# Kernel tuning notes

Hardware: AMD Instinct MI355X
Metric: run time of the kernel (lower is better)

The kernel has to match this reference:

```python
import jax, jax.numpy as jnp
import numpy as np

EMBED_DIM = 1024
B, T = 4, 2048

def setup_inputs() -> dict:
    key = jax.random.key(0)
    ks = jax.random.split(key, 7)
    s = 1.0 / np.sqrt(EMBED_DIM)
    return {
        "x": jax.random.normal(ks[0], (B, T, EMBED_DIM), dtype=jnp.float32),
        "Wq": jax.random.uniform(ks[1], (EMBED_DIM, EMBED_DIM), jnp.float32, -s, s),
        "bq": jax.random.uniform(ks[2], (EMBED_DIM,), jnp.float32, -s, s),
        "Wk": jax.random.uniform(ks[3], (EMBED_DIM, EMBED_DIM), jnp.float32, -s, s),
        "bk": jax.random.uniform(ks[4], (EMBED_DIM,), jnp.float32, -s, s),
        "Wv": jax.random.uniform(ks[5], (EMBED_DIM, EMBED_DIM), jnp.float32, -s, s),
        "bv": jax.random.uniform(ks[6], (EMBED_DIM,), jnp.float32, -s, s),
    }

def reference(x, Wq, bq, Wk, bk, Wv, bv):
    Bsz, Tlen, C = x.shape
    # torch Linear: y = x @ W.T + b
    Q = jnp.einsum('btc,dc->btd', x, Wq) + bq
    K = jnp.einsum('btc,dc->btd', x, Wk) + bk
    V = jnp.einsum('btc,dc->btd', x, Wv) + bv
    score = jnp.einsum('bqd,bkd->bqk', Q, K) / jnp.sqrt(jnp.float32(C))
    causal = jnp.tril(jnp.ones((Tlen, Tlen), dtype=bool))  # [T,T]
    score = jnp.where(causal, score, -jnp.inf)
    att = jax.nn.softmax(score, axis=-1)
    return jnp.einsum('bqk,bkd->bqd', att, V)
```

## Files before the change

kernel.cpp:

```cpp
#include <hip/hip_runtime.h>


using u16 = unsigned short;
typedef __attribute__((ext_vector_type(8))) short short8;
typedef __attribute__((ext_vector_type(4))) float f32x4;

__device__ __forceinline__ u16 f2b(float f) {
  unsigned u = __builtin_bit_cast(unsigned, f);
  u += 0x7fffu + ((u >> 16) & 1u);
  return (u16)(u >> 16);
}

__device__ __forceinline__ float b2f(u16 h) {
  return __builtin_bit_cast(float, (unsigned)h << 16);
}

__device__ __forceinline__ void async16(void* lds, const void* g) {
  __builtin_amdgcn_global_load_lds(
      (const __attribute__((address_space(1))) unsigned int*)g,
      (__attribute__((address_space(3))) unsigned int*)lds, 16, 0, 0);
}

__device__ __forceinline__ void block_barrier() {
  asm volatile("" ::: "memory");
  __builtin_amdgcn_s_barrier();
  asm volatile("" ::: "memory");
}

__global__ __launch_bounds__(256) void cvt_all_kernel(
    const float* __restrict__ x, const float* __restrict__ Wq,
    const float* __restrict__ Wk, const float* __restrict__ Wv,
    u16* __restrict__ xb, u16* __restrict__ Wcat) {
  const int i = blockIdx.x * 256 + threadIdx.x;
  const float* src;
  u16* dst;
  int c;
  if (i < 2097152) {
    src = x; dst = xb; c = i;
  } else {
    const int r = i - 2097152;
    const int seg = r >> 18;
    src = seg == 0 ? Wq : (seg == 1 ? Wk : Wv);
    dst = Wcat + (size_t)seg * 1048576;
    c = r & 262143;
  }
  const float4 v = reinterpret_cast<const float4*>(src)[c];
  ushort4 o;
  o.x = f2b(v.x); o.y = f2b(v.y); o.z = f2b(v.z); o.w = f2b(v.w);
  reinterpret_cast<ushort4*>(dst)[c] = o;
}

#define STG_A(buf, half, roff, ku)                                          \
  {                                                                         \
    async16(&Asm[buf][half][tid * 8], gA0 + (size_t)(roff)*lda + (ku));     \
    async16(&Asm[buf][half][4096 + tid * 8],                                \
            gA0 + (size_t)((roff) + 128) * lda + (ku));                     \
  }
#define STG_B(buf, half, roff, ku)                                          \
  {                                                                         \
    async16(&Bsm[buf][half][tid * 8], gB0 + (size_t)(roff)*ldb + (ku));     \
    async16(&Bsm[buf][half][4096 + tid * 8],                                \
            gB0 + (size_t)((roff) + 128) * ldb + (ku));                     \
  }
#define RD_A(buf, hh)                                                       \
  {                                                                         \
    _Pragma("unroll") for (int ii = 0; ii < 4; ++ii) {                      \
      a[ii][0] = *(const short8*)(&Asm[buf][hh][aoff + ii * 1024 + sk0]);   \
      a[ii][1] = *(const short8*)(&Asm[buf][hh][aoff + ii * 1024 + sk1]);   \
    }                                                                       \
  }
#define RD_B(buf, cc, breg)                                                 \
  {                                                                         \
    _Pragma("unroll") for (int jj = 0; jj < 2; ++jj) {                      \
      breg[jj][0] = *(const short8*)(&Bsm[buf][cc][boff + jj * 1024 + sk0]);\
      breg[jj][1] = *(const short8*)(&Bsm[buf][cc][boff + jj * 1024 + sk1]);\
    }                                                                       \
  }
#define QUAD(hh, cc, breg)                                                  \
  {                                                                         \
    __builtin_amdgcn_s_setprio(1);                                          \
    _Pragma("unroll") for (int ii = 0; ii < 4; ++ii)                        \
        _Pragma("unroll") for (int jj = 0; jj < 2; ++jj) {                  \
      acc[(hh)*4 + ii][(cc)*2 + jj] =                                       \
          __builtin_amdgcn_mfma_f32_16x16x32_bf16(                          \
              a[ii][0], breg[jj][0], acc[(hh)*4 + ii][(cc)*2 + jj], 0,0,0); \
      acc[(hh)*4 + ii][(cc)*2 + jj] =                                       \
          __builtin_amdgcn_mfma_f32_16x16x32_bf16(                          \
              a[ii][1], breg[jj][1], acc[(hh)*4 + ii][(cc)*2 + jj], 0,0,0); \
    }                                                                       \
    __builtin_amdgcn_s_setprio(0);                                          \
  }
#define LGK0 asm volatile("s_waitcnt lgkmcnt(0)" ::: "memory")
#define LGK8 asm volatile("s_waitcnt lgkmcnt(8)" ::: "memory")
#define VM6 asm volatile("s_waitcnt vmcnt(6)" ::: "memory")

template <int NT, typename Epi>
__device__ __forceinline__ void gemm256_8ph(const u16* __restrict__ A, int lda,
                                            const u16* __restrict__ B, int ldb,
                                            Epi&& epi) {
  __shared__ __align__(16) u16 Asm[2][2][8192];
  __shared__ __align__(16) u16 Bsm[2][2][8192];
  const int tid = threadIdx.x;
  const int lane = tid & 63;
  const int w = tid >> 6;
  const int wm = w >> 2;
  const int wn = w & 3;

  f32x4 acc[8][4];
#pragma unroll
  for (int i = 0; i < 8; ++i)
#pragma unroll
    for (int j = 0; j < 4; ++j) acc[i][j] = f32x4{0.f, 0.f, 0.f, 0.f};

  const int sr = tid >> 3;
  const int ce = ((tid & 7) ^ (sr & 7)) << 3;
  const u16* gA0 = A + (size_t)sr * lda + ce;
  const int bE = (sr & 31) + ((sr >> 5) << 6);
  const u16* gB0 = B + (size_t)bE * ldb + ce;

  const int l15 = lane & 15;
  const int hi = lane >> 4;
  const int lo7 = lane & 7;
  const int aoff = wm * 4096 + l15 * 64;
  const int boff = wn * 2048 + l15 * 64;
  const int sk0 = (hi ^ lo7) << 3;
  const int sk1 = ((4 + hi) ^ lo7) << 3;

  short8 a[4][2], bEr[2][2], bLr[2][2];

  STG_A(0, 0, 0, 0); STG_B(0, 0, 0, 0); STG_A(0, 1, 64, 0); STG_B(0, 1, 32, 0);
  STG_A(1, 0, 0, 64); STG_B(1, 0, 0, 64); STG_A(1, 1, 64, 64);
  VM6;
  block_barrier();

  for (int t = 0; t < NT; t += 2) {
    const int k1 = (t + 1) * 64;
    const int t2c = (t + 2 < NT) ? (t + 2) : (NT - 1);
    const int t3c = (t + 3 < NT) ? (t + 3) : (NT - 1);
    const int k2 = t2c * 64;
    const int k3 = t3c * 64;
    RD_A(0, 0); RD_B(0, 0, bEr); STG_B(1, 1, 32, k1); LGK8;
    block_barrier(); LGK0; QUAD(0, 0, bEr); block_barrier();
    RD_B(0, 1, bLr); STG_A(0, 0, 0, k2);
    block_barrier(); LGK0; QUAD(0, 1, bLr); block_barrier();
    RD_A(0, 1); STG_B(0, 0, 0, k2);
    block_barrier(); LGK0; QUAD(1, 1, bLr); block_barrier();
    STG_A(0, 1, 64, k2);
    VM6; block_barrier(); QUAD(1, 0, bEr); block_barrier();
    RD_A(1, 0); RD_B(1, 0, bEr); STG_B(0, 1, 32, k2); LGK8;
    block_barrier(); LGK0; QUAD(0, 0, bEr); block_barrier();
    RD_B(1, 1, bLr); STG_A(1, 0, 0, k3);
    block_barrier(); LGK0; QUAD(0, 1, bLr); block_barrier();
    RD_A(1, 1); STG_B(1, 0, 0, k3);
    block_barrier(); LGK0; QUAD(1, 1, bLr); block_barrier();
    STG_A(1, 1, 64, k3);
    VM6; block_barrier(); QUAD(1, 0, bEr); block_barrier();
  }
  asm volatile("s_waitcnt vmcnt(0)" ::: "memory");
  epi(acc, wm, wn, lane);
}

__global__ __launch_bounds__(512, 1) void qkv_qk_kernel(
    const u16* __restrict__ xb, const u16* __restrict__ Wcat,
    const float* __restrict__ bq, const float* __restrict__ bk,
    u16* __restrict__ Qb, u16* __restrict__ Kb) {
  const int bid = blockIdx.x;
  const int swz = (bid & 7) * 32 + (bid >> 3);
  const int mt = swz >> 3, nt = swz & 7;
  const int z = nt >> 2;
  const float* bias = z ? bk : bq;
  u16* out = z ? Kb : Qb;
  const float scale = z ? 1.0f : 0.03125f;
  gemm256_8ph<16>(
      xb + (size_t)mt * 256 * 1024, 1024, Wcat + (size_t)nt * 256 * 1024, 1024,
      [&](f32x4(&acc)[8][4], int wm, int wn, int lane) {
        const int r0 = mt * 256 + wm * 128 + ((lane >> 4) << 2);
        const int c0 = (nt & 3) * 256 + wn * 64 + (lane & 15);
#pragma unroll
        for (int i8 = 0; i8 < 8; ++i8) {
          const int rb = r0 + (i8 >> 2) * 64 + (i8 & 3) * 16;
#pragma unroll
          for (int i4 = 0; i4 < 4; ++i4) {
            const int col = c0 + (i4 >> 1) * 32 + (i4 & 1) * 16;
            const float bb = bias[col];
#pragma unroll
            for (int rr = 0; rr < 4; ++rr)
              out[(size_t)(rb + rr) * 1024 + col] =
                  f2b((acc[i8][i4][rr] + bb) * scale);
          }
        }
      });
}

template <typename Epi>
__device__ __forceinline__ void gemm_bt_tile(const u16* __restrict__ A, int lda,
                                             const u16* __restrict__ B, int ldb,
                                             int nt, Epi&& epi) {
  __shared__ __align__(16) u16 As[128 * 64];
  __shared__ __align__(16) u16 Bs[128 * 64];
  const int tid = threadIdx.x;
  const int lane = tid & 63;
  const int w = tid >> 6;
  const int wr = (w >> 1) << 6;
  const int wc = (w & 1) << 6;

  f32x4 acc[4][4];
#pragma unroll
  for (int i = 0; i < 4; ++i)
#pragma unroll
    for (int j = 0; j < 4; ++j) acc[i][j] = f32x4{0.f, 0.f, 0.f, 0.f};

  const int sr = tid >> 3;
  const int ce = ((tid & 7) ^ (sr & 7)) << 3;
  const u16* gA = A + (size_t)sr * lda + ce;
  const u16* gB = B + (size_t)sr * ldb + ce;
  u16* const dA = As + tid * 8;
  u16* const dB = Bs + tid * 8;

  const int hi = lane >> 4;
  const int lo7 = lane & 7;
  const int ra = (wr + (lane & 15)) << 6;
  const int rb = (wc + (lane & 15)) << 6;
  const int sk0 = (hi ^ lo7) << 3;
  const int sk1 = ((4 + hi) ^ lo7) << 3;

  for (int t = 0; t < nt; ++t) {
    __syncthreads();
#pragma unroll
    for (int s = 0; s < 4; ++s) {
      async16(dA + s * 2048, gA + (size_t)(s * 32) * lda);
      async16(dB + s * 2048, gB + (size_t)(s * 32) * ldb);
    }
    gA += 64;
    gB += 64;
    __syncthreads();
#pragma unroll
    for (int kk = 0; kk < 2; ++kk) {
      const int sk = kk ? sk1 : sk0;
      short8 af[4], bf[4];
#pragma unroll
      for (int i = 0; i < 4; ++i)
        af[i] = *(const short8*)(As + ra + i * 1024 + sk);
#pragma unroll
      for (int j = 0; j < 4; ++j)
        bf[j] = *(const short8*)(Bs + rb + j * 1024 + sk);
#pragma unroll
      for (int i = 0; i < 4; ++i)
#pragma unroll
        for (int j = 0; j < 4; ++j)
          acc[i][j] = __builtin_amdgcn_mfma_f32_16x16x32_bf16(af[i], bf[j],
                                                              acc[i][j], 0, 0, 0);
    }
  }
  epi(acc, wr, wc, lane);
}

template <typename Epi>
__device__ __forceinline__ void gemm_bt_128k(const u16* __restrict__ A, int lda,
                                             const u16* __restrict__ B, int ldb,
                                             int nt, Epi&& epi) {
  __shared__ __align__(16) u16 As[2][128 * 64];
  __shared__ __align__(16) u16 Bs[2][128 * 64];
  const int tid = threadIdx.x;
  const int lane = tid & 63;
  const int w = tid >> 6;
  const int wr = (w >> 1) << 6;
  const int wc = (w & 1) << 6;

  f32x4 acc[4][4];
#pragma unroll
  for (int i = 0; i < 4; ++i)
#pragma unroll
    for (int j = 0; j < 4; ++j) acc[i][j] = f32x4{0.f, 0.f, 0.f, 0.f};

  const int sr = tid >> 3;
  const int ce = ((tid & 7) ^ (sr & 7)) << 3;
  const u16* gA = A + (size_t)sr * lda + ce;
  const u16* gB = B + (size_t)sr * ldb + ce;

  const int hi = lane >> 4;
  const int lo7 = lane & 7;
  const int ra = (wr + (lane & 15)) << 6;
  const int rb = (wc + (lane & 15)) << 6;
  const int sk0 = (hi ^ lo7) << 3;
  const int sk1 = ((4 + hi) ^ lo7) << 3;

  for (int t = 0; t < nt; ++t) {
    __syncthreads();
#pragma unroll
    for (int kh = 0; kh < 2; ++kh)
#pragma unroll
      for (int s = 0; s < 4; ++s) {
        async16(&As[kh][tid * 8 + s * 2048],
                gA + kh * 64 + (size_t)(s * 32) * lda);
        async16(&Bs[kh][tid * 8 + s * 2048],
                gB + kh * 64 + (size_t)(s * 32) * ldb);
      }
    gA += 128;
    gB += 128;
    __syncthreads();
#pragma unroll
    for (int kk = 0; kk < 4; ++kk) {
      const int kh = kk >> 1;
      const int sk = (kk & 1) ? sk1 : sk0;
      short8 af[4], bf[4];
#pragma unroll
      for (int i = 0; i < 4; ++i)
        af[i] = *(const short8*)(&As[kh][ra + i * 1024 + sk]);
#pragma unroll
      for (int j = 0; j < 4; ++j)
        bf[j] = *(const short8*)(&Bs[kh][rb + j * 1024 + sk]);
#pragma unroll
      for (int i = 0; i < 4; ++i)
#pragma unroll
        for (int j = 0; j < 4; ++j)
          acc[i][j] = __builtin_amdgcn_mfma_f32_16x16x32_bf16(af[i], bf[j],
                                                              acc[i][j], 0, 0, 0);
    }
  }
  epi(acc, wr, wc, lane);
}

__global__ __launch_bounds__(256) void qkv_v_kernel(
    const u16* __restrict__ xb, const u16* __restrict__ Wcat,
    const float* __restrict__ bv, u16* __restrict__ Vtb) {
  const int bid = blockIdx.x;
  const int u = bid >> 3;
  const int nt = (bid & 7) * 8 + (u >> 3);
  const int mt = u & 7;
  const u16* Wvb = Wcat + (size_t)2 * 1048576;
  gemm_bt_tile(
      Wvb + (size_t)mt * 128 * 1024, 1024, xb + (size_t)nt * 128 * 1024, 1024, 16,
      [&](f32x4(&acc)[4][4], int wr, int wc, int lane) {
        const int r0 = mt * 128 + wr + ((lane >> 4) << 2);
        const int c0 = nt * 128 + wc + (lane & 15);
#pragma unroll
        for (int i = 0; i < 4; ++i)
#pragma unroll
          for (int rr = 0; rr < 4; ++rr) {
            const int row = r0 + i * 16 + rr;
            const float bb = bv[row];
#pragma unroll
            for (int j = 0; j < 4; ++j)
              Vtb[(size_t)row * 8192 + c0 + j * 16] = f2b(acc[i][j][rr] + bb);
          }
      });
}

__global__ __launch_bounds__(256) void score_kernel(const u16* __restrict__ Qb,
                                                    const u16* __restrict__ Kb,
                                                    u16* __restrict__ S) {
  const int b = blockIdx.y;
  const int traw = blockIdx.x;
  const int t = (traw & 7) * 17 + (traw >> 3);
  int qt = 0;
  while ((qt + 1) * (qt + 2) / 2 <= t) ++qt;
  const int kt = t - (qt * (qt + 1)) / 2;
  const u16* A = Qb + ((size_t)b * 2048 + qt * 128) * 1024;
  const u16* Bp = Kb + ((size_t)b * 2048 + kt * 128) * 1024;
  u16* Sb = S + (size_t)b * 2048 * 2048;
  gemm_bt_tile(A, 1024, Bp, 1024, 16,
               [&](f32x4(&acc)[4][4], int wr, int wc, int lane) {
                 const int r0 = qt * 128 + wr + ((lane >> 4) << 2);
                 const int c0 = kt * 128 + wc + (lane & 15);
#pragma unroll
                 for (int i = 0; i < 4; ++i)
#pragma unroll
                   for (int j = 0; j < 4; ++j)
#pragma unroll
                     for (int rr = 0; rr < 4; ++rr)
                       Sb[(size_t)(r0 + i * 16 + rr) * 2048 + c0 + j * 16] =
                           f2b(acc[i][j][rr]);
               });
}

__global__ __launch_bounds__(256) void softmax_kernel(const u16* __restrict__ S,
                                                      u16* __restrict__ P) {
  __shared__ float redm[4], reds[4];
  const int rowid = blockIdx.x;
  const int b = rowid >> 11;
  const int q = rowid & 2047;
  const u16* Srow = S + ((size_t)b * 2048 + q) * 2048;
  u16* Prow = P + ((size_t)b * 2048 + q) * 2048;
  const int L = q + 1;
  const int Lpad = ((q >> 7) + 1) << 7;
  const int tid = threadIdx.x;
  const int k0 = tid << 3;
  const bool active = k0 < Lpad;
  float v[8];
  float m = -1e30f;
  if (active) {
    const short8 s8 = *(const short8*)(Srow + k0);
#pragma unroll
    for (int j = 0; j < 8; ++j) {
      v[j] = (k0 + j < L) ? b2f((u16)s8[j]) : -1e30f;
      m = fmaxf(m, v[j]);
    }
  }
#pragma unroll
  for (int o = 32; o > 0; o >>= 1) m = fmaxf(m, __shfl_xor(m, o));
  if ((tid & 63) == 0) redm[tid >> 6] = m;
  __syncthreads();
  m = fmaxf(fmaxf(redm[0], redm[1]), fmaxf(redm[2], redm[3]));
  float s = 0.f;
  if (active) {
#pragma unroll
    for (int j = 0; j < 8; ++j) {
      const float e = (k0 + j < L) ? __expf(v[j] - m) : 0.f;
      v[j] = e;
      s += e;
    }
  }
#pragma unroll
  for (int o = 32; o > 0; o >>= 1) s += __shfl_xor(s, o);
  if ((tid & 63) == 0) reds[tid >> 6] = s;
  __syncthreads();
  s = reds[0] + reds[1] + reds[2] + reds[3];
  const float inv = 1.0f / s;
  if (active) {
    short8 o8;
#pragma unroll
    for (int j = 0; j < 8; ++j)
      o8[j] = (short)((k0 + j < L) ? f2b(v[j] * inv) : (u16)0);
    *(short8*)(Prow + k0) = o8;
  }
}

__global__ __launch_bounds__(256) void pv_kernel(const u16* __restrict__ P,
                                                 const u16* __restrict__ Vtb,
                                                 float* __restrict__ O) {
  const int bid = blockIdx.x;
  const int g = bid >> 5;
  const int qt = (g & 1) ? ((g - 1) >> 1) : (15 - (g >> 1));
  const int inner = bid & 31;
  const int b = inner >> 3;
  const int dt = inner & 7;
  const u16* A = P + (size_t)b * 2048 * 2048 + (size_t)qt * 128 * 2048;
  const u16* Bp = Vtb + (size_t)dt * 128 * 8192 + b * 2048;
  float* Ob = O + (size_t)b * 2048 * 1024;
  gemm_bt_128k(A, 2048, Bp, 8192, qt + 1,
               [&](f32x4(&acc)[4][4], int wr, int wc, int lane) {
                 const int r0 = qt * 128 + wr + ((lane >> 4) << 2);
                 const int c0 = dt * 128 + wc + (lane & 15);
#pragma unroll
                 for (int i = 0; i < 4; ++i)
#pragma unroll
                   for (int j = 0; j < 4; ++j)
#pragma unroll
                     for (int rr = 0; rr < 4; ++rr)
                       Ob[(size_t)(r0 + i * 16 + rr) * 1024 + c0 + j * 16] =
                           acc[i][j][rr];
               });
}

extern "C" void kernel_launch(void* const* d_in, const int* in_sizes, int n_in,
                              void* d_out, int out_size, void* d_ws, size_t ws_size,
                              hipStream_t stream) {
  const float* x = (const float*)d_in[0];
  const float* Wq = (const float*)d_in[1];
  const float* bq = (const float*)d_in[2];
  const float* Wk = (const float*)d_in[3];
  const float* bk = (const float*)d_in[4];
  const float* Wv = (const float*)d_in[5];
  const float* bv = (const float*)d_in[6];
  float* out = (float*)d_out;
  char* ws = (char*)d_ws;
  u16* Qb = (u16*)(ws);
  u16* Kb = (u16*)(ws + (16u << 20));
  u16* Vtb = (u16*)(ws + (32u << 20));
  u16* xb = (u16*)(ws + (48u << 20));
  u16* Wcat = (u16*)(ws + (64u << 20));
  u16* S = (u16*)(ws + (70u << 20));
  u16* P = (u16*)(ws + (134u << 20));

  cvt_all_kernel<<<11264, 256, 0, stream>>>(x, Wq, Wk, Wv, xb, Wcat);
  qkv_qk_kernel<<<256, 512, 0, stream>>>(xb, Wcat, bq, bk, Qb, Kb);
  qkv_v_kernel<<<512, 256, 0, stream>>>(xb, Wcat, bv, Vtb);
  score_kernel<<<dim3(136, 4), 256, 0, stream>>>(Qb, Kb, S);
  softmax_kernel<<<8192, 256, 0, stream>>>(S, P);
  pv_kernel<<<512, 256, 0, stream>>>(P, Vtb, out);
}
```

Before: 150.6 us.

## Fuse causal softmax into PV GEMM with online-softmax rescaling

Removes the separate softmax kernel and the P buffer. The PV kernel now reads bf16 scores straight from S, computes exponentials with a running max and sum per row (online softmax), writes P tiles into LDS and rescales the accumulators each K-tile. The next S tile is prefetched into registers. This avoids a full write and reread of P plus one launch. In exchange, exp work is repeated for each of the 8 d-tiles and extra rescale math and barriers sit on the GEMM critical path.

```diff
diff --git a/kernel.cpp b/kernel.cpp
--- a/kernel.cpp
+++ b/kernel.cpp
@@ -255,72 +255,6 @@
   epi(acc, wr, wc, lane);
 }
 
-template <typename Epi>
-__device__ __forceinline__ void gemm_bt_128k(const u16* __restrict__ A, int lda,
-                                             const u16* __restrict__ B, int ldb,
-                                             int nt, Epi&& epi) {
-  __shared__ __align__(16) u16 As[2][128 * 64];
-  __shared__ __align__(16) u16 Bs[2][128 * 64];
-  const int tid = threadIdx.x;
-  const int lane = tid & 63;
-  const int w = tid >> 6;
-  const int wr = (w >> 1) << 6;
-  const int wc = (w & 1) << 6;
-
-  f32x4 acc[4][4];
-#pragma unroll
-  for (int i = 0; i < 4; ++i)
-#pragma unroll
-    for (int j = 0; j < 4; ++j) acc[i][j] = f32x4{0.f, 0.f, 0.f, 0.f};
-
-  const int sr = tid >> 3;
-  const int ce = ((tid & 7) ^ (sr & 7)) << 3;
-  const u16* gA = A + (size_t)sr * lda + ce;
-  const u16* gB = B + (size_t)sr * ldb + ce;
-
-  const int hi = lane >> 4;
-  const int lo7 = lane & 7;
-  const int ra = (wr + (lane & 15)) << 6;
-  const int rb = (wc + (lane & 15)) << 6;
-  const int sk0 = (hi ^ lo7) << 3;
-  const int sk1 = ((4 + hi) ^ lo7) << 3;
-
-  for (int t = 0; t < nt; ++t) {
-    __syncthreads();
-#pragma unroll
-    for (int kh = 0; kh < 2; ++kh)
-#pragma unroll
-      for (int s = 0; s < 4; ++s) {
-        async16(&As[kh][tid * 8 + s * 2048],
-                gA + kh * 64 + (size_t)(s * 32) * lda);
-        async16(&Bs[kh][tid * 8 + s * 2048],
-                gB + kh * 64 + (size_t)(s * 32) * ldb);
-      }
-    gA += 128;
-    gB += 128;
-    __syncthreads();
-#pragma unroll
-    for (int kk = 0; kk < 4; ++kk) {
-      const int kh = kk >> 1;
-      const int sk = (kk & 1) ? sk1 : sk0;
-      short8 af[4], bf[4];
-#pragma unroll
-      for (int i = 0; i < 4; ++i)
-        af[i] = *(const short8*)(&As[kh][ra + i * 1024 + sk]);
-#pragma unroll
-      for (int j = 0; j < 4; ++j)
-        bf[j] = *(const short8*)(&Bs[kh][rb + j * 1024 + sk]);
-#pragma unroll
-      for (int i = 0; i < 4; ++i)
-#pragma unroll
-        for (int j = 0; j < 4; ++j)
-          acc[i][j] = __builtin_amdgcn_mfma_f32_16x16x32_bf16(af[i], bf[j],
-                                                              acc[i][j], 0, 0, 0);
-    }
-  }
-  epi(acc, wr, wc, lane);
-}
-
 __global__ __launch_bounds__(256) void qkv_v_kernel(
     const u16* __restrict__ xb, const u16* __restrict__ Wcat,
     const float* __restrict__ bv, u16* __restrict__ Vtb) {
@@ -374,83 +308,151 @@
                });
 }
 
-__global__ __launch_bounds__(256) void softmax_kernel(const u16* __restrict__ S,
-                                                      u16* __restrict__ P) {
-  __shared__ float redm[4], reds[4];
-  const int rowid = blockIdx.x;
-  const int b = rowid >> 11;
-  const int q = rowid & 2047;
-  const u16* Srow = S + ((size_t)b * 2048 + q) * 2048;
-  u16* Prow = P + ((size_t)b * 2048 + q) * 2048;
-  const int L = q + 1;
-  const int Lpad = ((q >> 7) + 1) << 7;
-  const int tid = threadIdx.x;
-  const int k0 = tid << 3;
-  const bool active = k0 < Lpad;
-  float v[8];
-  float m = -1e30f;
-  if (active) {
-    const short8 s8 = *(const short8*)(Srow + k0);
-#pragma unroll
-    for (int j = 0; j < 8; ++j) {
-      v[j] = (k0 + j < L) ? b2f((u16)s8[j]) : -1e30f;
-      m = fmaxf(m, v[j]);
-    }
-  }
-#pragma unroll
-  for (int o = 32; o > 0; o >>= 1) m = fmaxf(m, __shfl_xor(m, o));
-  if ((tid & 63) == 0) redm[tid >> 6] = m;
-  __syncthreads();
-  m = fmaxf(fmaxf(redm[0], redm[1]), fmaxf(redm[2], redm[3]));
-  float s = 0.f;
-  if (active) {
-#pragma unroll
-    for (int j = 0; j < 8; ++j) {
-      const float e = (k0 + j < L) ? __expf(v[j] - m) : 0.f;
-      v[j] = e;
-      s += e;
-    }
-  }
-#pragma unroll
-  for (int o = 32; o > 0; o >>= 1) s += __shfl_xor(s, o);
-  if ((tid & 63) == 0) reds[tid >> 6] = s;
-  __syncthreads();
-  s = reds[0] + reds[1] + reds[2] + reds[3];
-  const float inv = 1.0f / s;
-  if (active) {
-    short8 o8;
-#pragma unroll
-    for (int j = 0; j < 8; ++j)
-      o8[j] = (short)((k0 + j < L) ? f2b(v[j] * inv) : (u16)0);
-    *(short8*)(Prow + k0) = o8;
-  }
-}
-
-__global__ __launch_bounds__(256) void pv_kernel(const u16* __restrict__ P,
-                                                 const u16* __restrict__ Vtb,
-                                                 float* __restrict__ O) {
+__global__ __launch_bounds__(256) void spv_kernel(const u16* __restrict__ S,
+                                                  const u16* __restrict__ Vtb,
+                                                  float* __restrict__ O) {
+  __shared__ __align__(16) u16 Pl[2][128 * 64];
+  __shared__ __align__(16) u16 Bl[2][128 * 64];
+  __shared__ float scale_lds[128];
+  __shared__ float l_lds[128];
+
   const int bid = blockIdx.x;
   const int g = bid >> 5;
   const int qt = (g & 1) ? ((g - 1) >> 1) : (15 - (g >> 1));
   const int inner = bid & 31;
   const int b = inner >> 3;
   const int dt = inner & 7;
-  const u16* A = P + (size_t)b * 2048 * 2048 + (size_t)qt * 128 * 2048;
-  const u16* Bp = Vtb + (size_t)dt * 128 * 8192 + b * 2048;
+
+  const int tid = threadIdx.x;
+  const int lane = tid & 63;
+  const int w = tid >> 6;
+  const int wr = (w >> 1) << 6;
+  const int wc = (w & 1) << 6;
+
+  f32x4 acc[4][4];
+#pragma unroll
+  for (int i = 0; i < 4; ++i)
+#pragma unroll
+    for (int j = 0; j < 4; ++j) acc[i][j] = f32x4{0.f, 0.f, 0.f, 0.f};
+
+  const int trow = w * 32 + (lane >> 1);
+  const int tch = lane & 1;
+  const u16* Srow =
+      S + ((size_t)b * 2048 + qt * 128 + trow) * 2048 + tch * 64;
+  u16* const pwr = &Pl[tch][trow * 64];
+  const int rsw = trow & 7;
+
+  const int sr = tid >> 3;
+  const int ce = ((tid & 7) ^ (sr & 7)) << 3;
+  const u16* gB =
+      Vtb + (size_t)dt * 128 * 8192 + (size_t)b * 2048 + (size_t)sr * 8192 + ce;
+
+  const int hi = lane >> 4;
+  const int lo7 = lane & 7;
+  const int ra = (wr + (lane & 15)) << 6;
+  const int rb = (wc + (lane & 15)) << 6;
+  const int sk0 = (hi ^ lo7) << 3;
+  const int sk1 = ((4 + hi) ^ lo7) << 3;
+
+  float m_run = -1e30f, l_run = 0.f;
+  const int NT = qt + 1;
+
+  short8 sCur[8], sNxt[8];
+#pragma unroll
+  for (int c = 0; c < 8; ++c) sCur[c] = *(const short8*)(Srow + c * 8);
+
+  for (int kt = 0; kt < NT; ++kt) {
+    const u16* gBk = gB + kt * 128;
+#pragma unroll
+    for (int kh = 0; kh < 2; ++kh)
+#pragma unroll
+      for (int s = 0; s < 4; ++s)
+        async16(&Bl[kh][tid * 8 + s * 2048],
+                gBk + kh * 64 + (size_t)(s * 32) * 8192);
+    const bool diag = (kt == qt);
+    float tmax = -1e30f;
+#pragma unroll
+    for (int c = 0; c < 8; ++c)
+#pragma unroll
+      for (int j = 0; j < 8; ++j) {
+        float v = b2f((u16)sCur[c][j]);
+        if (diag && (tch * 64 + c * 8 + j) > trow) v = -1e30f;
+        tmax = fmaxf(tmax, v);
+      }
+    tmax = fmaxf(tmax, __shfl_xor(tmax, 1));
+    const float m_new = fmaxf(m_run, tmax);
+    const float sc = __expf(m_run - m_new);
+    m_run = m_new;
+    float lsum = 0.f;
+#pragma unroll
+    for (int c = 0; c < 8; ++c) {
+      short8 o8;
+#pragma unroll
+      for (int j = 0; j < 8; ++j) {
+        const float v = b2f((u16)sCur[c][j]);
+        const float e = (diag && (tch * 64 + c * 8 + j) > trow)
+                            ? 0.f
+                            : __expf(v - m_new);
+        lsum += e;
+        o8[j] = (short)f2b(e);
+      }
+      *(short8*)(pwr + ((c ^ rsw) << 3)) = o8;
+    }
+    lsum += __shfl_xor(lsum, 1);
+    l_run = l_run * sc + lsum;
+    if ((lane & 1) == 0) scale_lds[trow] = sc;
+    const int ktn = (kt + 1 < NT) ? (kt + 1) : kt;
+#pragma unroll
+    for (int c = 0; c < 8; ++c)
+      sNxt[c] = *(const short8*)(Srow + ktn * 128 + c * 8);
+    asm volatile("s_waitcnt lgkmcnt(0)" ::: "memory");
+    asm volatile("s_waitcnt vmcnt(8)" ::: "memory");
+    __builtin_amdgcn_s_barrier();
+#pragma unroll
+    for (int i = 0; i < 4; ++i)
+#pragma unroll
+      for (int rr = 0; rr < 4; ++rr) {
+        const float s_ = scale_lds[wr + i * 16 + 4 * hi + rr];
+#pragma unroll
+        for (int j = 0; j < 4; ++j) acc[i][j][rr] *= s_;
+      }
+#pragma unroll
+    for (int kk = 0; kk < 4; ++kk) {
+      const int kh = kk >> 1;
+      const int sk = (kk & 1) ? sk1 : sk0;
+      short8 af[4], bf[4];
+#pragma unroll
+      for (int i = 0; i < 4; ++i)
+        af[i] = *(const short8*)(&Pl[kh][ra + i * 1024 + sk]);
+#pragma unroll
+      for (int j = 0; j < 4; ++j)
+        bf[j] = *(const short8*)(&Bl[kh][rb + j * 1024 + sk]);
+#pragma unroll
+      for (int i = 0; i < 4; ++i)
+#pragma unroll
+        for (int j = 0; j < 4; ++j)
+          acc[i][j] = __builtin_amdgcn_mfma_f32_16x16x32_bf16(af[i], bf[j],
+                                                              acc[i][j], 0, 0, 0);
+    }
+    block_barrier();
+#pragma unroll
+    for (int c = 0; c < 8; ++c) sCur[c] = sNxt[c];
+  }
+  if ((lane & 1) == 0) l_lds[trow] = l_run;
+  __syncthreads();
   float* Ob = O + (size_t)b * 2048 * 1024;
-  gemm_bt_128k(A, 2048, Bp, 8192, qt + 1,
-               [&](f32x4(&acc)[4][4], int wr, int wc, int lane) {
-                 const int r0 = qt * 128 + wr + ((lane >> 4) << 2);
-                 const int c0 = dt * 128 + wc + (lane & 15);
-#pragma unroll
-                 for (int i = 0; i < 4; ++i)
-#pragma unroll
-                   for (int j = 0; j < 4; ++j)
-#pragma unroll
-                     for (int rr = 0; rr < 4; ++rr)
-                       Ob[(size_t)(r0 + i * 16 + rr) * 1024 + c0 + j * 16] =
-                           acc[i][j][rr];
-               });
+  const int r0 = qt * 128 + wr + (hi << 2);
+  const int c0 = dt * 128 + wc + (lane & 15);
+#pragma unroll
+  for (int i = 0; i < 4; ++i)
+#pragma unroll
+    for (int rr = 0; rr < 4; ++rr) {
+      const float il = 1.0f / l_lds[wr + i * 16 + 4 * hi + rr];
+#pragma unroll
+      for (int j = 0; j < 4; ++j)
+        Ob[(size_t)(r0 + i * 16 + rr) * 1024 + c0 + j * 16] =
+            acc[i][j][rr] * il;
+    }
 }
 
 extern "C" void kernel_launch(void* const* d_in, const int* in_sizes, int n_in,
@@ -471,12 +473,10 @@
   u16* xb = (u16*)(ws + (48u << 20));
   u16* Wcat = (u16*)(ws + (64u << 20));
   u16* S = (u16*)(ws + (70u << 20));
-  u16* P = (u16*)(ws + (134u << 20));
 
   cvt_all_kernel<<<11264, 256, 0, stream>>>(x, Wq, Wk, Wv, xb, Wcat);
   qkv_qk_kernel<<<256, 512, 0, stream>>>(xb, Wcat, bq, bk, Qb, Kb);
   qkv_v_kernel<<<512, 256, 0, stream>>>(xb, Wcat, bv, Vtb);
   score_kernel<<<dim3(136, 4), 256, 0, stream>>>(Qb, Kb, S);
-  softmax_kernel<<<8192, 256, 0, stream>>>(S, P);
-  pv_kernel<<<512, 256, 0, stream>>>(P, Vtb, out);
-}
+  spv_kernel<<<512, 256, 0, stream>>>(S, Vtb, out);
+}
```

New measurement: 186.2 us. +23.7%, slower.
